# Optimization experiments

Hardware: AMD Instinct MI355X
Metric: run time of the kernel (lower is better)

Reference implementation:

```python
import jax, jax.numpy as jnp
import numpy as np

EPS = 1e-08
N_NODES = 100000
E_HALF = 3200000  # directed edges before symmetrization


def setup_inputs() -> dict:
    key = jax.random.key(0)
    k1, k2, k3 = jax.random.split(key, 3)
    pos = jax.random.normal(k1, (N_NODES, 3), dtype=jnp.float32)
    phi = jax.random.normal(k2, (N_NODES,), dtype=jnp.float32)
    e = jax.random.randint(k3, (2, E_HALF), 0, N_NODES, dtype=jnp.int32)
    # symmetrize (the torch module calls to_undirected); build undirected edge list
    edge_index = jnp.concatenate([e, e[::-1]], axis=1)  # (2, 2*E_HALF)
    return {"pos": pos, "phi": phi, "edge_index": edge_index}


def reference(pos, phi, edge_index):
    # pos: (N, 3), phi: (N,), edge_index: (2, E) already undirected
    n = pos.shape[0]
    row, col = edge_index[0], edge_index[1]
    dx = pos[col] - pos[row]                      # (E, 3)
    dphi = phi[col] - phi[row]                    # (E,)
    w = 1.0 / (jnp.linalg.norm(dx, axis=1) + EPS) ** 2  # (E,)
    outer = dx[:, :, None] * dx[:, None, :]      # (E, 3, 3)
    A = jax.ops.segment_sum(w[:, None, None] * outer, row, num_segments=n)  # (N,3,3)
    b = jax.ops.segment_sum((w * dphi)[:, None] * dx, row, num_segments=n)  # (N,3)
    A_reg = A + EPS * jnp.eye(3, dtype=pos.dtype)[None, :, :]
    grad_phi = jnp.linalg.solve(A_reg, b[..., None])[..., 0]  # (N,3)
    return grad_phi
```

## Files before the change

### kernel.cpp

```cpp
#include <hip/hip_runtime.h>
#include <hip/hip_bf16.h>
#include <math.h>

#define LSQ_EPS 1e-8f
#define BUCKET_BITS 8
#define BUCKET_SIZE 256
#define NB_MAX 400
#define CAP 17408
#define SCAT_BLOCKS 1024
#define STAGE_CAP 6272
#define VEC_ITERS 4
#define KV 9

__device__ __forceinline__ int hget(const unsigned int* hp, int b) {
    return (int)((hp[b >> 1] >> ((b & 1) * 16)) & 0xFFFFu);
}
__device__ __forceinline__ unsigned int hinc_rank(unsigned int* hp, int b) {
    unsigned int o = atomicAdd(&hp[b >> 1], 1u << ((b & 1) * 16));
    return (o >> ((b & 1) * 16)) & 0xFFFFu;
}

__global__ __launch_bounds__(256, 5) void lsq_scatter_sorted(
    const float* __restrict__ pos, const float* __restrict__ phi,
    const int* __restrict__ eidx, int E, int N, int NB,
    float4* __restrict__ pp4,
    unsigned int* __restrict__ region, int* __restrict__ g_cursor)
{
    __shared__ unsigned int staged[STAGE_CAP];
    __shared__ unsigned int histp[NB_MAX / 2];
    __shared__ unsigned short base16[NB_MAX];
    __shared__ unsigned short sstart16[NB_MAX];

    const int tid = threadIdx.x;
    const int E2 = E >> 1;

    for (int i = blockIdx.x * 256 + tid; i < N; i += SCAT_BLOCKS * 256)
        pp4[i] = make_float4(pos[3 * i + 0], pos[3 * i + 1], pos[3 * i + 2], phi[i]);

    int chunk = (E2 + SCAT_BLOCKS - 1) / SCAT_BLOCKS;
    chunk = (chunk + 3) & ~3;
    const int start = blockIdx.x * chunk;
    const int end = min(start + chunk, E2);
    if (start >= E2) return;

    for (int t = tid; t < NB_MAX / 2; t += 256) histp[t] = 0;
    __syncthreads();

    const int nvec = (end - start) & ~3;
    unsigned int rkA[VEC_ITERS][4];
    int4 rA[VEC_ITERS], cA[VEC_ITERS];
#pragma unroll
    for (int k = 0; k < VEC_ITERS; ++k) {
        int e = start + (tid << 2) + (k << 10);
        if (e < start + nvec) {
            int4 r = *(const int4*)(eidx + e);
            int4 c = *(const int4*)(eidx + E + e);
            rA[k] = r;
            cA[k] = c;
            rkA[k][0] = hinc_rank(histp, r.x >> BUCKET_BITS) |
                        (hinc_rank(histp, c.x >> BUCKET_BITS) << 16);
            rkA[k][1] = hinc_rank(histp, r.y >> BUCKET_BITS) |
                        (hinc_rank(histp, c.y >> BUCKET_BITS) << 16);
            rkA[k][2] = hinc_rank(histp, r.z >> BUCKET_BITS) |
                        (hinc_rank(histp, c.z >> BUCKET_BITS) << 16);
            rkA[k][3] = hinc_rank(histp, r.w >> BUCKET_BITS) |
                        (hinc_rank(histp, c.w >> BUCKET_BITS) << 16);
        }
    }
    unsigned int rkT = 0;
    int trow = 0, tcol = 0;
    const int tcnt = (end - start) - nvec;
    if (tid < tcnt) {
        int e = start + nvec + tid;
        trow = eidx[e];
        tcol = eidx[E + e];
        rkT = hinc_rank(histp, trow >> BUCKET_BITS) |
              (hinc_rank(histp, tcol >> BUCKET_BITS) << 16);
    }
    __syncthreads();

    int bs0 = 0, bs1 = 0;
    {
        int b = tid;
        if (b < NB) { int c = hget(histp, b); if (c > 0) bs0 = atomicAdd(&g_cursor[b], c); }
        b += 256;
        if (b < NB) { int c = hget(histp, b); if (c > 0) bs1 = atomicAdd(&g_cursor[b], c); }
    }
    if (tid < 64) {
        int carry = 0;
        for (int bi = 0; bi < NB; bi += 64) {
            int b = bi + tid;
            int c = (b < NB) ? hget(histp, b) : 0;
            int x = c;
#pragma unroll
            for (int d = 1; d < 64; d <<= 1) {
                int y = __shfl_up(x, d, 64);
                if (tid >= d) x += y;
            }
            if (b < NB) sstart16[b] = (unsigned short)(carry + x - c);
            carry += __shfl(x, 63, 64);
        }
    }
    asm volatile("s_waitcnt lgkmcnt(0)" ::: "memory");
    __builtin_amdgcn_s_barrier();

#pragma unroll
    for (int k = 0; k < VEC_ITERS; ++k) {
        int e = start + (tid << 2) + (k << 10);
        if (e < start + nvec) {
            int rr[4] = {rA[k].x, rA[k].y, rA[k].z, rA[k].w};
            int cc[4] = {cA[k].x, cA[k].y, cA[k].z, cA[k].w};
#pragma unroll
            for (int q = 0; q < 4; ++q) {
                int b1 = rr[q] >> BUCKET_BITS;
                int s1 = (int)sstart16[b1] + (int)(rkA[k][q] & 0xFFFFu);
                staged[s1] = ((unsigned int)(rr[q] & (BUCKET_SIZE - 1)) << 17) | (unsigned int)cc[q];
                int b2 = cc[q] >> BUCKET_BITS;
                int s2 = (int)sstart16[b2] + (int)(rkA[k][q] >> 16);
                staged[s2] = ((unsigned int)(cc[q] & (BUCKET_SIZE - 1)) << 17) | (unsigned int)rr[q];
            }
        }
    }
    if (tid < tcnt) {
        int b1 = trow >> BUCKET_BITS;
        staged[(int)sstart16[b1] + (int)(rkT & 0xFFFFu)] =
            ((unsigned int)(trow & (BUCKET_SIZE - 1)) << 17) | (unsigned int)tcol;
        int b2 = tcol >> BUCKET_BITS;
        staged[(int)sstart16[b2] + (int)(rkT >> 16)] =
            ((unsigned int)(tcol & (BUCKET_SIZE - 1)) << 17) | (unsigned int)trow;
    }

    if (tid < NB)       base16[tid]       = (unsigned short)min(bs0, 65535);
    if (tid + 256 < NB) base16[tid + 256] = (unsigned short)min(bs1, 65535);
    __syncthreads();

    {
        const int wv = tid >> 6, ln = tid & 63;
        const int grp = ln >> 4;
        const int sub = ln & 15;
        for (int b = wv * 4 + grp; b < NB; b += 16) {
            int cnt_b = hget(histp, b);
            if (cnt_b == 0) continue;
            int src = (int)sstart16[b];
            int dst = (int)base16[b];
            int kmax = min(cnt_b, CAP - dst);
            if (kmax <= 0) continue;
            unsigned int* dstp = region + (size_t)b * CAP + dst;
            const unsigned int* srcp = staged + src;
            for (int j = sub; j < kmax; j += 16)
                dstp[j] = srcp[j];
        }
    }
}

#define LSQ_ACC(qv)                                                            \
    {                                                                          \
        float dx = (qv).x - me.x;                                              \
        float dy = (qv).y - me.y;                                              \
        float dz = (qv).z - me.z;                                              \
        float dphi = (qv).w - me.w;                                            \
        float nn = sqrtf(dx * dx + dy * dy + dz * dz) + LSQ_EPS;               \
        float w = 1.0f / (nn * nn);                                            \
        float wd = w * dphi;                                                   \
        a00 += w * dx * dx; a01 += w * dx * dy; a02 += w * dx * dz;            \
        a11 += w * dy * dy; a12 += w * dy * dz; a22 += w * dz * dz;            \
        bb0 += wd * dx;     bb1 += wd * dy;     bb2 += wd * dz;                \
    }

__global__ __launch_bounds__(512, 4) void lsq_bucket_reduce(
    const float4* __restrict__ pp4,
    const unsigned int* __restrict__ region, const int* __restrict__ g_cursor,
    float* __restrict__ out, int N)
{
    __shared__ unsigned int sorted32[CAP];
    __shared__ int cnt[BUCKET_SIZE];
    __shared__ int startx[BUCKET_SIZE];

    const int b = blockIdx.x;
    const int tid = threadIdx.x;
    const int node_base = b << BUCKET_BITS;

    if (tid < BUCKET_SIZE) cnt[tid] = 0;
    __syncthreads();

    int count = g_cursor[b];
    if (count > CAP) count = CAP;
    const unsigned int* reg = region + (size_t)b * CAP;

    uint4 pcv[KV];
#pragma unroll
    for (int k = 0; k < KV; ++k) {
        int i = (tid << 2) + (k << 11);
        if (i < count) {
            uint4 p = *(const uint4*)(reg + i);
            unsigned int o0 = (unsigned int)atomicAdd(&cnt[p.x >> 17], 1);
            pcv[k].x = p.x | (o0 << 25);
            if (i + 1 < count) {
                unsigned int o1 = (unsigned int)atomicAdd(&cnt[p.y >> 17], 1);
                pcv[k].y = p.y | (o1 << 25);
            }
            if (i + 2 < count) {
                unsigned int o2 = (unsigned int)atomicAdd(&cnt[p.z >> 17], 1);
                pcv[k].z = p.z | (o2 << 25);
            }
            if (i + 3 < count) {
                unsigned int o3 = (unsigned int)atomicAdd(&cnt[p.w >> 17], 1);
                pcv[k].w = p.w | (o3 << 25);
            }
        }
    }
    __syncthreads();

    if (tid < 64) {
        int carry = 0;
        for (int base = 0; base < BUCKET_SIZE; base += 64) {
            int c = cnt[base + tid];
            int x = c;
#pragma unroll
            for (int d = 1; d < 64; d <<= 1) {
                int y = __shfl_up(x, d, 64);
                if (tid >= d) x += y;
            }
            startx[base + tid] = carry + x - c;
            carry += __shfl(x, 63, 64);
        }
    }
    __syncthreads();

#pragma unroll
    for (int k = 0; k < KV; ++k) {
        int i = (tid << 2) + (k << 11);
        if (i < count) {
            unsigned int p0 = pcv[k].x;
            sorted32[startx[(p0 >> 17) & 0xFFu] + (int)(p0 >> 25)] = p0 & 0x1FFFFu;
            if (i + 1 < count) {
                unsigned int p1 = pcv[k].y;
                sorted32[startx[(p1 >> 17) & 0xFFu] + (int)(p1 >> 25)] = p1 & 0x1FFFFu;
            }
            if (i + 2 < count) {
                unsigned int p2 = pcv[k].z;
                sorted32[startx[(p2 >> 17) & 0xFFu] + (int)(p2 >> 25)] = p2 & 0x1FFFFu;
            }
            if (i + 3 < count) {
                unsigned int p3 = pcv[k].w;
                sorted32[startx[(p3 >> 17) & 0xFFu] + (int)(p3 >> 25)] = p3 & 0x1FFFFu;
            }
        }
    }
    __syncthreads();

    const int n = tid >> 1;
    const int qid = tid & 1;
    int node = node_base + n;
    float4 me = pp4[node < N ? node : 0];
    const int s = startx[n];
    const int cN = cnt[n];
    int lo = s + (cN * qid) / 2;
    const int hi = s + (cN * (qid + 1)) / 2;

    float a00 = 0, a01 = 0, a02 = 0, a11 = 0, a12 = 0, a22 = 0;
    float bb0 = 0, bb1 = 0, bb2 = 0;

    int i = lo;
    for (; i + 3 < hi; i += 4) {
        int c0 = (int)sorted32[i];
        int c1 = (int)sorted32[i + 1];
        int c2 = (int)sorted32[i + 2];
        int c3 = (int)sorted32[i + 3];
        float4 q0 = pp4[c0];
        float4 q1 = pp4[c1];
        float4 q2 = pp4[c2];
        float4 q3 = pp4[c3];
        LSQ_ACC(q0); LSQ_ACC(q1); LSQ_ACC(q2); LSQ_ACC(q3);
    }
    for (; i < hi; ++i) {
        int c0 = (int)sorted32[i];
        float4 q0 = pp4[c0];
        LSQ_ACC(q0);
    }

    a00 += __shfl_down(a00, 1); a01 += __shfl_down(a01, 1);
    a02 += __shfl_down(a02, 1); a11 += __shfl_down(a11, 1);
    a12 += __shfl_down(a12, 1); a22 += __shfl_down(a22, 1);
    bb0 += __shfl_down(bb0, 1); bb1 += __shfl_down(bb1, 1);
    bb2 += __shfl_down(bb2, 1);

    if (qid == 0 && node < N) {
        double a00d = (double)a00 + 1e-8;
        double a01d = (double)a01;
        double a02d = (double)a02;
        double a11d = (double)a11 + 1e-8;
        double a12d = (double)a12;
        double a22d = (double)a22 + 1e-8;
        double b0 = (double)bb0;
        double b1 = (double)bb1;
        double b2 = (double)bb2;

        double c00 = a11d * a22d - a12d * a12d;
        double c01 = a02d * a12d - a01d * a22d;
        double c02 = a01d * a12d - a02d * a11d;
        double c11 = a00d * a22d - a02d * a02d;
        double c12 = a01d * a02d - a00d * a12d;
        double c22 = a00d * a11d - a01d * a01d;

        double det = a00d * c00 + a01d * c01 + a02d * c02;
        double inv = 1.0 / det;

        out[node * 3 + 0] = (float)((c00 * b0 + c01 * b1 + c02 * b2) * inv);
        out[node * 3 + 1] = (float)((c01 * b0 + c11 * b1 + c12 * b2) * inv);
        out[node * 3 + 2] = (float)((c02 * b0 + c12 * b1 + c22 * b2) * inv);
    }
}

__global__ void lsq_edge_scatter(const float* __restrict__ pos,
                                 const float* __restrict__ phi,
                                 const int* __restrict__ eidx,
                                 float* __restrict__ acc,
                                 int E) {
    int e = blockIdx.x * blockDim.x + threadIdx.x;
    if (e >= E) return;
    int r = eidx[e];
    int c = eidx[E + e];
    float dx = pos[3 * c + 0] - pos[3 * r + 0];
    float dy = pos[3 * c + 1] - pos[3 * r + 1];
    float dz = pos[3 * c + 2] - pos[3 * r + 2];
    float dphi = phi[c] - phi[r];
    float n = sqrtf(dx * dx + dy * dy + dz * dz) + LSQ_EPS;
    float w = 1.0f / (n * n);
    float wd = w * dphi;
    float* a = acc + (size_t)r * 9;
    unsafeAtomicAdd(a + 0, w * dx * dx);
    unsafeAtomicAdd(a + 1, w * dx * dy);
    unsafeAtomicAdd(a + 2, w * dx * dz);
    unsafeAtomicAdd(a + 3, w * dy * dy);
    unsafeAtomicAdd(a + 4, w * dy * dz);
    unsafeAtomicAdd(a + 5, w * dz * dz);
    unsafeAtomicAdd(a + 6, wd * dx);
    unsafeAtomicAdd(a + 7, wd * dy);
    unsafeAtomicAdd(a + 8, wd * dz);
}

__global__ void lsq_solve3(const float* __restrict__ acc,
                           float* __restrict__ out,
                           int N) {
    int i = blockIdx.x * blockDim.x + threadIdx.x;
    if (i >= N) return;
    const float* a = acc + (size_t)i * 9;
    double a00 = (double)a[0] + 1e-8;
    double a01 = (double)a[1];
    double a02 = (double)a[2];
    double a11 = (double)a[3] + 1e-8;
    double a12 = (double)a[4];
    double a22 = (double)a[5] + 1e-8;
    double b0 = (double)a[6];
    double b1 = (double)a[7];
    double b2 = (double)a[8];
    double c00 = a11 * a22 - a12 * a12;
    double c01 = a02 * a12 - a01 * a22;
    double c02 = a01 * a12 - a02 * a11;
    double c11 = a00 * a22 - a02 * a02;
    double c12 = a01 * a02 - a00 * a12;
    double c22 = a00 * a11 - a01 * a01;
    double det = a00 * c00 + a01 * c01 + a02 * c02;
    double inv = 1.0 / det;
    out[3 * i + 0] = (float)((c00 * b0 + c01 * b1 + c02 * b2) * inv);
    out[3 * i + 1] = (float)((c01 * b0 + c11 * b1 + c12 * b2) * inv);
    out[3 * i + 2] = (float)((c02 * b0 + c12 * b1 + c22 * b2) * inv);
}

extern "C" void kernel_launch(void* const* d_in, const int* in_sizes, int n_in,
                              void* d_out, int out_size, void* d_ws, size_t ws_size,
                              hipStream_t stream) {
    const float* pos = (const float*)d_in[0];
    const float* phi = (const float*)d_in[1];
    const int* eidx = (const int*)d_in[2];
    float* out = (float*)d_out;

    int N = in_sizes[0] / 3;
    int E = in_sizes[2] / 2;
    int NB = (N + BUCKET_SIZE - 1) >> BUCKET_BITS;

    size_t region_bytes = (size_t)NB * CAP * sizeof(unsigned int);
    size_t pp4_bytes = (size_t)N * sizeof(float4);
    size_t need = region_bytes + pp4_bytes + (size_t)NB * sizeof(int);

    int chunk = ((E / 2) + SCAT_BLOCKS - 1) / SCAT_BLOCKS;
    chunk = (chunk + 3) & ~3;
    bool stage_ok = (2 * chunk) <= STAGE_CAP;

    if (NB <= NB_MAX && ws_size >= need && (E & 3) == 0 && stage_ok) {
        unsigned int* region = (unsigned int*)d_ws;
        float4* pp4 = (float4*)((char*)d_ws + region_bytes);
        int* g_cursor = (int*)((char*)d_ws + region_bytes + pp4_bytes);

        hipMemsetAsync(g_cursor, 0, (size_t)NB * sizeof(int), stream);
        lsq_scatter_sorted<<<SCAT_BLOCKS, 256, 0, stream>>>(
            pos, phi, eidx, E, N, NB, pp4, region, g_cursor);
        lsq_bucket_reduce<<<NB, 512, 0, stream>>>(pp4, region, g_cursor, out, N);
    } else {
        float* acc = (float*)d_ws;
        hipMemsetAsync(acc, 0, (size_t)N * 9 * sizeof(float), stream);
        int threads = 256;
        lsq_edge_scatter<<<(E + threads - 1) / threads, threads, 0, stream>>>(pos, phi, eidx, acc, E);
        lsq_solve3<<<(N + threads - 1) / threads, threads, 0, stream>>>(acc, out, N);
    }
}
```

Before: 163.8 us.

## Double node bucket size to 512 and use 1024-thread reduce blocks

Each bucket now covers 512 nodes instead of 256, which halves the bucket count and the per-block global cursor atomics in the scatter kernel. The reduce kernel now runs 1024 threads per block and keeps a per-edge rank table of twice the size in LDS. Because the wider local node index overlaps the old rank bit field, the per-edge ranks are moved into a separate packed 8-bit register array. The trade-off is that only about 196 large blocks are launched, which may leave many of the GPU's CUs idle. Each block also needs about 137 KB of LDS, leaving little headroom per CU.

```diff
diff --git a/kernel.cpp b/kernel.cpp
--- a/kernel.cpp
+++ b/kernel.cpp
@@ -3,10 +3,10 @@
 #include <math.h>
 
 #define LSQ_EPS 1e-8f
-#define BUCKET_BITS 8
-#define BUCKET_SIZE 256
-#define NB_MAX 400
-#define CAP 17408
+#define BUCKET_BITS 9
+#define BUCKET_SIZE 512
+#define NB_MAX 200
+#define CAP 34304
 #define SCAT_BLOCKS 1024
 #define STAGE_CAP 6272
 #define VEC_ITERS 4
@@ -79,12 +79,10 @@
     }
     __syncthreads();
 
-    int bs0 = 0, bs1 = 0;
-    {
-        int b = tid;
-        if (b < NB) { int c = hget(histp, b); if (c > 0) bs0 = atomicAdd(&g_cursor[b], c); }
-        b += 256;
-        if (b < NB) { int c = hget(histp, b); if (c > 0) bs1 = atomicAdd(&g_cursor[b], c); }
+    int bs0 = 0;
+    if (tid < NB) {
+        int c = hget(histp, tid);
+        if (c > 0) bs0 = atomicAdd(&g_cursor[tid], c);
     }
     if (tid < 64) {
         int carry = 0;
@@ -130,8 +128,7 @@
             ((unsigned int)(tcol & (BUCKET_SIZE - 1)) << 17) | (unsigned int)trow;
     }
 
-    if (tid < NB)       base16[tid]       = (unsigned short)min(bs0, 65535);
-    if (tid + 256 < NB) base16[tid + 256] = (unsigned short)min(bs1, 65535);
+    if (tid < NB) base16[tid] = (unsigned short)min(bs0, 65535);
     __syncthreads();
 
     {
@@ -167,7 +164,7 @@
         bb0 += wd * dx;     bb1 += wd * dy;     bb2 += wd * dz;                \
     }
 
-__global__ __launch_bounds__(512, 4) void lsq_bucket_reduce(
+__global__ __launch_bounds__(1024, 4) void lsq_bucket_reduce(
     const float4* __restrict__ pp4,
     const unsigned int* __restrict__ region, const int* __restrict__ g_cursor,
     float* __restrict__ out, int N)
@@ -188,24 +185,27 @@
     const unsigned int* reg = region + (size_t)b * CAP;
 
     uint4 pcv[KV];
+    unsigned int prk[KV];
 #pragma unroll
     for (int k = 0; k < KV; ++k) {
-        int i = (tid << 2) + (k << 11);
+        int i = (tid << 2) + (k << 12);
+        prk[k] = 0;
         if (i < count) {
             uint4 p = *(const uint4*)(reg + i);
+            pcv[k] = p;
             unsigned int o0 = (unsigned int)atomicAdd(&cnt[p.x >> 17], 1);
-            pcv[k].x = p.x | (o0 << 25);
+            prk[k] = (o0 & 0xFFu);
             if (i + 1 < count) {
                 unsigned int o1 = (unsigned int)atomicAdd(&cnt[p.y >> 17], 1);
-                pcv[k].y = p.y | (o1 << 25);
+                prk[k] |= (o1 & 0xFFu) << 8;
             }
             if (i + 2 < count) {
                 unsigned int o2 = (unsigned int)atomicAdd(&cnt[p.z >> 17], 1);
-                pcv[k].z = p.z | (o2 << 25);
+                prk[k] |= (o2 & 0xFFu) << 16;
             }
             if (i + 3 < count) {
                 unsigned int o3 = (unsigned int)atomicAdd(&cnt[p.w >> 17], 1);
-                pcv[k].w = p.w | (o3 << 25);
+                prk[k] |= (o3 & 0xFFu) << 24;
             }
         }
     }
@@ -229,21 +229,21 @@
 
 #pragma unroll
     for (int k = 0; k < KV; ++k) {
-        int i = (tid << 2) + (k << 11);
+        int i = (tid << 2) + (k << 12);
         if (i < count) {
             unsigned int p0 = pcv[k].x;
-            sorted32[startx[(p0 >> 17) & 0xFFu] + (int)(p0 >> 25)] = p0 & 0x1FFFFu;
+            sorted32[startx[p0 >> 17] + (int)(prk[k] & 0xFFu)] = p0 & 0x1FFFFu;
             if (i + 1 < count) {
                 unsigned int p1 = pcv[k].y;
-                sorted32[startx[(p1 >> 17) & 0xFFu] + (int)(p1 >> 25)] = p1 & 0x1FFFFu;
+                sorted32[startx[p1 >> 17] + (int)((prk[k] >> 8) & 0xFFu)] = p1 & 0x1FFFFu;
             }
             if (i + 2 < count) {
                 unsigned int p2 = pcv[k].z;
-                sorted32[startx[(p2 >> 17) & 0xFFu] + (int)(p2 >> 25)] = p2 & 0x1FFFFu;
+                sorted32[startx[p2 >> 17] + (int)((prk[k] >> 16) & 0xFFu)] = p2 & 0x1FFFFu;
             }
             if (i + 3 < count) {
                 unsigned int p3 = pcv[k].w;
-                sorted32[startx[(p3 >> 17) & 0xFFu] + (int)(p3 >> 25)] = p3 & 0x1FFFFu;
+                sorted32[startx[p3 >> 17] + (int)(prk[k] >> 24)] = p3 & 0x1FFFFu;
             }
         }
     }
@@ -396,7 +396,7 @@
         hipMemsetAsync(g_cursor, 0, (size_t)NB * sizeof(int), stream);
         lsq_scatter_sorted<<<SCAT_BLOCKS, 256, 0, stream>>>(
             pos, phi, eidx, E, N, NB, pp4, region, g_cursor);
-        lsq_bucket_reduce<<<NB, 512, 0, stream>>>(pp4, region, g_cursor, out, N);
+        lsq_bucket_reduce<<<NB, 1024, 0, stream>>>(pp4, region, g_cursor, out, N);
     } else {
         float* acc = (float*)d_ws;
         hipMemsetAsync(acc, 0, (size_t)N * 9 * sizeof(float), stream);
```

After: 156.7 us. 4.3% less time.
